# Optimization experiments

Measured on AMD Instinct MI355X. Metric: run time of the kernel, lower is better.

The kernel has to match this reference:

```python
import jax, jax.numpy as jnp
import numpy as np

# dims: batch, seq, d_model, heads, n_buckets, n_hashes, d_ff
B, S, D, H, NB, R, DFF = 2, 4096, 1024, 16, 64, 4, 4096
DH = D // H          # head dim
C = S // NB          # attention chunk length after bucket sort
NCH = S // C         # number of chunks


def layernorm(x, g, b):
    m = x.mean(-1, keepdims=True)
    v = ((x - m) ** 2).mean(-1, keepdims=True)
    return (x - m) / jnp.sqrt(v + 1e-5) * g + b


def lsh_attention(x, Wqk, Wv, Wo, rot):
    Bx, Sx, _ = x.shape
    # shared QK projection (Reformer-style), separate V
    qk = (x @ Wqk).reshape(Bx, Sx, H, DH).transpose(0, 2, 1, 3)  # [B,H,S,dh]
    v = (x @ Wv).reshape(Bx, Sx, H, DH).transpose(0, 2, 1, 3)
    # random-rotation LSH: rot [dh, R, NB//2]
    rotated = jnp.einsum('bhsd,drk->rbhsk', qk, rot)
    buckets = jnp.argmax(jnp.concatenate([rotated, -rotated], -1), -1)  # [R,B,H,S]
    scale = DH ** -0.5
    pos = jnp.arange(Sx)

    def one_round(b_r):  # b_r: [B,H,S] bucket ids for one hash round
        order = jnp.argsort(b_r * Sx + pos, axis=-1)   # stable sort by bucket
        inv = jnp.argsort(order, axis=-1)
        sqk = jnp.take_along_axis(qk, order[..., None], 2)
        sv = jnp.take_along_axis(v, order[..., None], 2)
        sb = jnp.take_along_axis(b_r, order, -1)
        q_c = sqk.reshape(Bx, H, NCH, C, DH)
        # keys are L2-normalized shared qk
        k_c = (sqk / (jnp.linalg.norm(sqk, axis=-1, keepdims=True) + 1e-6)).reshape(Bx, H, NCH, C, DH)
        v_c = sv.reshape(Bx, H, NCH, C, DH)
        ext = lambda t: jnp.concatenate([t, jnp.roll(t, 1, axis=2)], axis=3)  # look back 1 chunk
        k_e, v_e = ext(k_c), ext(v_c)
        b_c = sb.reshape(Bx, H, NCH, C)
        b_e = jnp.concatenate([b_c, jnp.roll(b_c, 1, axis=2)], 3)
        p_c = order.reshape(Bx, H, NCH, C)
        p_e = jnp.concatenate([p_c, jnp.roll(p_c, 1, axis=2)], 3)
        s = jnp.einsum('bhnqd,bhnkd->bhnqk', q_c, k_e) * scale  # [B,H,nch,C,2C]
        s = jnp.where(b_c[..., :, None] == b_e[..., None, :], s, -1e9)   # only same bucket
        s = jnp.where(p_c[..., :, None] == p_e[..., None, :], -1e5, s)   # discourage self
        l = jax.scipy.special.logsumexp(s, -1)
        o = jnp.einsum('bhnqk,bhnkd->bhnqd', jax.nn.softmax(s, -1), v_e)
        o = o.reshape(Bx, H, Sx, DH)
        l = l.reshape(Bx, H, Sx)
        return jnp.take_along_axis(o, inv[..., None], 2), jnp.take_along_axis(l, inv, -1)

    o_all, l_all = jax.vmap(one_round)(buckets)        # [R,B,H,S,dh], [R,B,H,S]
    w = jax.nn.softmax(l_all, axis=0)[..., None]       # weight rounds by logsumexp
    out = (o_all * w).sum(0).transpose(0, 2, 1, 3).reshape(Bx, Sx, D)
    return out @ Wo


def feedforward(x, W1, b1, W2, b2):
    # chunked FF in the original only tiles the sequence dim; math is identical
    return jax.nn.relu(x @ W1 + b1) @ W2 + b2


def setup_inputs() -> dict:
    key = jax.random.key(0)
    ks = jax.random.split(key, 10)
    n = jax.random.normal
    return {
        'x1': n(ks[0], (B, S, D), jnp.float32),
        'x2': n(ks[1], (B, S, D), jnp.float32),
        'Wqk': n(ks[2], (D, D), jnp.float32) * (D ** -0.5),
        'Wv': n(ks[3], (D, D), jnp.float32) * (D ** -0.5),
        'Wo': n(ks[4], (D, D), jnp.float32) * (D ** -0.5),
        'ln1_g': jnp.ones(D, jnp.float32), 'ln1_b': jnp.zeros(D, jnp.float32),
        'W1': n(ks[5], (D, DFF), jnp.float32) * (D ** -0.5), 'bf1': jnp.zeros(DFF, jnp.float32),
        'W2': n(ks[6], (DFF, D), jnp.float32) * (DFF ** -0.5), 'bf2': jnp.zeros(D, jnp.float32),
        'ln2_g': jnp.ones(D, jnp.float32), 'ln2_b': jnp.zeros(D, jnp.float32),
        'rot': n(ks[7], (DH, R, NB // 2), jnp.float32),
    }


def reference(x1, x2, Wqk, Wv, Wo, ln1_g, ln1_b, W1, bf1, W2, bf2, ln2_g, ln2_b, rot):
    # reversible block: y1 = x1 + Attn(LN(x2)); y2 = x2 + FF(LN(y1))
    y1 = x1 + lsh_attention(layernorm(x2, ln1_g, ln1_b), Wqk, Wv, Wo, rot)
    y2 = x2 + feedforward(layernorm(y1, ln2_g, ln2_b), W1, bf1, W2, bf2)
    return (y1, y2)
```

## Files before the change

kernel.cpp:

```cpp
#include <hip/hip_runtime.h>
#include <hip/hip_bf16.h>
#include <math.h>

constexpr int CB   = 2;
constexpr int CS   = 4096;
constexpr int CD   = 1024;
constexpr int CH   = 16;
constexpr int CDH  = 64;
constexpr int CR   = 4;
constexpr int CC   = 64;
constexpr int CNCH = 64;
constexpr int CDFF = 4096;
constexpr int CBS  = CB * CS;
constexpr int CBHS = CB * CH * CS;

typedef __attribute__((ext_vector_type(8))) short short8;
typedef __attribute__((ext_vector_type(4))) short short4v;
typedef __attribute__((ext_vector_type(4))) float f32x4;

__device__ inline unsigned short f2bf(float f) {
    __bf16 h = (__bf16)f;
    union { __bf16 h; unsigned short u; } c; c.h = h;
    return c.u;
}
__device__ inline unsigned int cvt2(float a, float b) {
    return (unsigned int)f2bf(a) | ((unsigned int)f2bf(b) << 16);
}
__device__ inline float bf2f(unsigned short h) {
    union { float f; unsigned int u; } a; a.u = ((unsigned int)h) << 16; return a.f;
}

#define AS3 __attribute__((address_space(3)))
#define AS1 __attribute__((address_space(1)))
__device__ inline void gload16(const unsigned short* g, unsigned short* l) {
    __builtin_amdgcn_global_load_lds((const AS1 unsigned int*)g,
                                     (AS3 unsigned int*)l, 16, 0, 0);
}

__device__ inline short8 ld_short8_u(const unsigned short* p) {
    short4v a = *(const short4v*)p;
    short4v b = *(const short4v*)(p + 4);
    short8 r;
    r[0] = a[0]; r[1] = a[1]; r[2] = a[2]; r[3] = a[3];
    r[4] = b[0]; r[5] = b[1]; r[6] = b[2]; r[7] = b[3];
    return r;
}

__global__ __launch_bounds__(256) void ln_kernel(const float* __restrict__ x,
        const float* __restrict__ g, const float* __restrict__ bta,
        unsigned short* __restrict__ out16, unsigned short* __restrict__ out16lo) {
    int row = blockIdx.x;
    int t = threadIdx.x;
    const float* xr = x + (size_t)row * CD;
    float4 v = *(const float4*)(xr + t * 4);
    float s  = v.x + v.y + v.z + v.w;
    float ss = v.x * v.x + v.y * v.y + v.z * v.z + v.w * v.w;
    #pragma unroll
    for (int off = 1; off < 64; off <<= 1) {
        s  += __shfl_xor(s, off);
        ss += __shfl_xor(ss, off);
    }
    __shared__ float ws_[4], wss_[4];
    int wid = t >> 6;
    if ((t & 63) == 0) { ws_[wid] = s; wss_[wid] = ss; }
    __syncthreads();
    s  = ws_[0] + ws_[1] + ws_[2] + ws_[3];
    ss = wss_[0] + wss_[1] + wss_[2] + wss_[3];
    float mean = s * (1.0f / CD);
    float var  = ss * (1.0f / CD) - mean * mean;
    float rstd = rsqrtf(var + 1e-5f);
    float4 gv = *(const float4*)(g + t * 4);
    float4 bv = *(const float4*)(bta + t * 4);
    float4 o;
    o.x = (v.x - mean) * rstd * gv.x + bv.x;
    o.y = (v.y - mean) * rstd * gv.y + bv.y;
    o.z = (v.z - mean) * rstd * gv.z + bv.z;
    o.w = (v.w - mean) * rstd * gv.w + bv.w;
    ushort4 h; h.x = f2bf(o.x); h.y = f2bf(o.y); h.z = f2bf(o.z); h.w = f2bf(o.w);
    *(ushort4*)(out16 + (size_t)row * CD + t * 4) = h;
    if (out16lo) {
        ushort4 lo;
        lo.x = f2bf(o.x - bf2f(h.x)); lo.y = f2bf(o.y - bf2f(h.y));
        lo.z = f2bf(o.z - bf2f(h.z)); lo.w = f2bf(o.w - bf2f(h.w));
        *(ushort4*)(out16lo + (size_t)row * CD + t * 4) = lo;
    }
}

__global__ __launch_bounds__(256) void wtrans_kernel(const float* __restrict__ W,
        unsigned short* __restrict__ WT, unsigned short* __restrict__ WTlo,
        int K, int N) {
    __shared__ float tile[64][65];
    int n0 = blockIdx.x * 64, k0 = blockIdx.y * 64;
    int tid = threadIdx.x;
    int r = tid >> 4, c4 = tid & 15;
    #pragma unroll
    for (int it = 0; it < 4; ++it) {
        int row = r + it * 16;
        float4 v = *(const float4*)(W + (size_t)(k0 + row) * N + n0 + c4 * 4);
        tile[row][c4 * 4 + 0] = v.x; tile[row][c4 * 4 + 1] = v.y;
        tile[row][c4 * 4 + 2] = v.z; tile[row][c4 * 4 + 3] = v.w;
    }
    __syncthreads();
    #pragma unroll
    for (int it = 0; it < 4; ++it) {
        int nrow = r + it * 16;
        float f0 = tile[c4 * 4 + 0][nrow], f1 = tile[c4 * 4 + 1][nrow];
        float f2 = tile[c4 * 4 + 2][nrow], f3 = tile[c4 * 4 + 3][nrow];
        ushort4 h;
        h.x = f2bf(f0); h.y = f2bf(f1); h.z = f2bf(f2); h.w = f2bf(f3);
        *(ushort4*)(WT + (size_t)(n0 + nrow) * K + k0 + c4 * 4) = h;
        if (WTlo) {
            ushort4 lo;
            lo.x = f2bf(f0 - bf2f(h.x)); lo.y = f2bf(f1 - bf2f(h.y));
            lo.z = f2bf(f2 - bf2f(h.z)); lo.w = f2bf(f3 - bf2f(h.w));
            *(ushort4*)(WTlo + (size_t)(n0 + nrow) * K + k0 + c4 * 4) = lo;
        }
    }
}

template<int EPI, int BM, int BK>
__global__ __launch_bounds__(256) void gemm_bf16(const unsigned short* __restrict__ A,
        const unsigned short* __restrict__ BT, const float* __restrict__ bias,
        const float* __restrict__ res, void* __restrict__ outp,
        int M, int N, int K) {
    constexpr int NH  = BK / 32;
    constexpr int SA  = BM / 64;
    constexpr int MI2 = BM / 32;
    __shared__ __align__(16) unsigned short As[NH * BM * 32];
    __shared__ __align__(16) unsigned short Bs[NH * 128 * 32];
    int tid = threadIdx.x;
    int w = tid >> 6, l = tid & 63;
    int nwg = gridDim.x * gridDim.y;
    int lid = blockIdx.y * gridDim.x + blockIdx.x;
    if (!(nwg & 7)) lid = (lid & 7) * (nwg >> 3) + (lid >> 3);
    int m0 = (lid / gridDim.x) * BM, n0 = (lid % gridDim.x) * 128;
    int wm = (w >> 1) * (BM / 2), wn = (w & 1) * 64;

    const unsigned short* gA[SA]; const unsigned short* gB[2];
    unsigned short* ldsA[SA]; unsigned short* ldsB[2];
    int gchunk = (l & 3) ^ ((l >> 3) & 3);
    #pragma unroll
    for (int s = 0; s < SA; ++s) {
        int j = w * SA + s;
        int R = j * 16 + (l >> 2);
        gA[s] = A + (size_t)(m0 + R) * K + gchunk * 8;
        ldsA[s] = As + j * 512;
    }
    #pragma unroll
    for (int s = 0; s < 2; ++s) {
        int j = w * 2 + s;
        int R = j * 16 + (l >> 2);
        gB[s] = BT + (size_t)(n0 + R) * K + gchunk * 8;
        ldsB[s] = Bs + j * 512;
    }
    int p = (l >> 4) ^ (((l & 15) >> 1) & 3);
    int aoff = (wm + (l & 15)) * 32 + p * 8;
    int boff = (wn + (l & 15)) * 32 + p * 8;

    f32x4 acc[MI2][4];
    #pragma unroll
    for (int i = 0; i < MI2; i++)
        #pragma unroll
        for (int j = 0; j < 4; j++) acc[i][j] = (f32x4)(0.f);

    for (int k0 = 0; k0 < K; k0 += BK) {
        #pragma unroll
        for (int h = 0; h < NH; ++h) {
            #pragma unroll
            for (int s = 0; s < SA; ++s)
                gload16(gA[s] + k0 + h * 32, ldsA[s] + h * (BM * 32));
            gload16(gB[0] + k0 + h * 32, ldsB[0] + h * (128 * 32));
            gload16(gB[1] + k0 + h * 32, ldsB[1] + h * (128 * 32));
        }
        __syncthreads();
        #pragma unroll
        for (int h = 0; h < NH; ++h) {
            short8 af[MI2], bf[4];
            #pragma unroll
            for (int im = 0; im < MI2; ++im)
                af[im] = *(const short8*)(As + h * (BM * 32) + aoff + im * 512);
            #pragma unroll
            for (int in = 0; in < 4; ++in)
                bf[in] = *(const short8*)(Bs + h * (128 * 32) + boff + in * 512);
            #pragma unroll
            for (int im = 0; im < MI2; ++im)
                #pragma unroll
                for (int in = 0; in < 4; ++in)
                    acc[im][in] = __builtin_amdgcn_mfma_f32_16x16x32_bf16(
                        af[im], bf[in], acc[im][in], 0, 0, 0);
        }
        __syncthreads();
    }

    float bv[4];
    if (EPI == 1 || EPI == 2) {
        #pragma unroll
        for (int in = 0; in < 4; ++in) bv[in] = bias[n0 + wn + in * 16 + (l & 15)];
    }
    #pragma unroll
    for (int im = 0; im < MI2; ++im) {
        #pragma unroll
        for (int in = 0; in < 4; ++in) {
            int n = n0 + wn + in * 16 + (l & 15);
            #pragma unroll
            for (int r = 0; r < 4; ++r) {
                int m = m0 + wm + im * 16 + (l >> 4) * 4 + r;
                float v = acc[im][in][r];
                if (EPI == 1) {
                    v = fmaxf(v + bv[in], 0.f);
                    ((unsigned short*)outp)[(size_t)m * N + n] = f2bf(v);
                } else if (EPI == 5) {
                    ((unsigned short*)outp)[(size_t)m * N + n] = f2bf(v);
                } else {
                    if (EPI == 2) v += bv[in] + res[(size_t)m * N + n];
                    if (EPI == 3) v += res[(size_t)m * N + n];
                    ((float*)outp)[(size_t)m * N + n] = v;
                }
            }
        }
    }
}

template<int BM>
__global__ __launch_bounds__(256) void gemm_bf16split(
        const unsigned short* __restrict__ Ah, const unsigned short* __restrict__ Al,
        const unsigned short* __restrict__ BTh, const unsigned short* __restrict__ BTl,
        float* __restrict__ outp, unsigned short* __restrict__ out16,
        int M, int N, int K) {
    constexpr int SA  = BM / 64;
    constexpr int MI2 = BM / 32;
    __shared__ __align__(16) unsigned short Ash[BM * 32];
    __shared__ __align__(16) unsigned short Asl[BM * 32];
    __shared__ __align__(16) unsigned short Bsh[128 * 32];
    __shared__ __align__(16) unsigned short Bsl[128 * 32];
    int tid = threadIdx.x;
    int w = tid >> 6, l = tid & 63;
    int nwg = gridDim.x * gridDim.y;
    int lid = blockIdx.y * gridDim.x + blockIdx.x;
    if (!(nwg & 7)) lid = (lid & 7) * (nwg >> 3) + (lid >> 3);
    int m0 = (lid / gridDim.x) * BM, n0 = (lid % gridDim.x) * 128;
    int wm = (w >> 1) * (BM / 2), wn = (w & 1) * 64;

    size_t goffA[SA]; size_t goffB[2];
    unsigned short* ldsAh[SA]; unsigned short* ldsAl[SA];
    unsigned short* ldsBh[2]; unsigned short* ldsBl[2];
    int gchunk = (l & 3) ^ ((l >> 3) & 3);
    #pragma unroll
    for (int s = 0; s < SA; ++s) {
        int j = w * SA + s;
        int R = j * 16 + (l >> 2);
        goffA[s] = (size_t)(m0 + R) * K + gchunk * 8;
        ldsAh[s] = Ash + j * 512; ldsAl[s] = Asl + j * 512;
    }
    #pragma unroll
    for (int s = 0; s < 2; ++s) {
        int j = w * 2 + s;
        int R = j * 16 + (l >> 2);
        goffB[s] = (size_t)(n0 + R) * K + gchunk * 8;
        ldsBh[s] = Bsh + j * 512; ldsBl[s] = Bsl + j * 512;
    }
    int p = (l >> 4) ^ (((l & 15) >> 1) & 3);
    int aoff = (wm + (l & 15)) * 32 + p * 8;
    int boff = (wn + (l & 15)) * 32 + p * 8;

    f32x4 acc[MI2][4];
    #pragma unroll
    for (int i = 0; i < MI2; i++)
        #pragma unroll
        for (int j = 0; j < 4; j++) acc[i][j] = (f32x4)(0.f);

    for (int k0 = 0; k0 < K; k0 += 32) {
        #pragma unroll
        for (int s = 0; s < SA; ++s) {
            gload16(Ah + goffA[s] + k0, ldsAh[s]);
            gload16(Al + goffA[s] + k0, ldsAl[s]);
        }
        #pragma unroll
        for (int s = 0; s < 2; ++s) {
            gload16(BTh + goffB[s] + k0, ldsBh[s]);
            gload16(BTl + goffB[s] + k0, ldsBl[s]);
        }
        __syncthreads();
        short8 afh[MI2], afl[MI2], bfh[4], bfl[4];
        #pragma unroll
        for (int im = 0; im < MI2; ++im) {
            afh[im] = *(const short8*)(Ash + aoff + im * 512);
            afl[im] = *(const short8*)(Asl + aoff + im * 512);
        }
        #pragma unroll
        for (int in = 0; in < 4; ++in) {
            bfh[in] = *(const short8*)(Bsh + boff + in * 512);
            bfl[in] = *(const short8*)(Bsl + boff + in * 512);
        }
        #pragma unroll
        for (int im = 0; im < MI2; ++im)
            #pragma unroll
            for (int in = 0; in < 4; ++in) {
                acc[im][in] = __builtin_amdgcn_mfma_f32_16x16x32_bf16(
                    afh[im], bfh[in], acc[im][in], 0, 0, 0);
                acc[im][in] = __builtin_amdgcn_mfma_f32_16x16x32_bf16(
                    afl[im], bfh[in], acc[im][in], 0, 0, 0);
                acc[im][in] = __builtin_amdgcn_mfma_f32_16x16x32_bf16(
                    afh[im], bfl[in], acc[im][in], 0, 0, 0);
            }
        __syncthreads();
    }

    #pragma unroll
    for (int im = 0; im < MI2; ++im)
        #pragma unroll
        for (int in = 0; in < 4; ++in) {
            int n = n0 + wn + in * 16 + (l & 15);
            #pragma unroll
            for (int r = 0; r < 4; ++r) {
                int m = m0 + wm + im * 16 + (l >> 4) * 4 + r;
                float v = acc[im][in][r];
                outp[(size_t)m * N + n] = v;
                out16[(size_t)m * N + n] = f2bf(v);
            }
        }
}

template<int EPI>
__global__ __launch_bounds__(256) void gemm_f32(const float* __restrict__ A,
        const float* __restrict__ W, float* __restrict__ out,
        int M, int N, int K) {
    __shared__ __align__(16) float As[16][132];
    __shared__ __align__(16) float Bs[16][132];
    int tid = threadIdx.x;
    int n0 = blockIdx.x * 128;
    int m0 = blockIdx.y * 128;
    int ty = tid >> 4, tx = tid & 15;
    float acc[8][8];
    #pragma unroll
    for (int i = 0; i < 8; i++)
        #pragma unroll
        for (int j = 0; j < 8; j++) acc[i][j] = 0.f;

    for (int k0 = 0; k0 < K; k0 += 16) {
        #pragma unroll
        for (int it = 0; it < 2; ++it) {
            int f4 = tid + it * 256;
            int row = f4 >> 2, c4 = f4 & 3;
            float4 av = *(const float4*)(A + (size_t)(m0 + row) * K + k0 + c4 * 4);
            As[c4 * 4 + 0][row] = av.x;
            As[c4 * 4 + 1][row] = av.y;
            As[c4 * 4 + 2][row] = av.z;
            As[c4 * 4 + 3][row] = av.w;
        }
        #pragma unroll
        for (int it = 0; it < 2; ++it) {
            int f4 = tid + it * 256;
            int kr = f4 >> 5, c4 = f4 & 31;
            *(float4*)(&Bs[kr][c4 * 4]) =
                *(const float4*)(W + (size_t)(k0 + kr) * N + n0 + c4 * 4);
        }
        __syncthreads();
        #pragma unroll
        for (int kk = 0; kk < 16; ++kk) {
            float4 a0 = *(const float4*)(&As[kk][ty * 8]);
            float4 a1 = *(const float4*)(&As[kk][ty * 8 + 4]);
            float4 b0 = *(const float4*)(&Bs[kk][tx * 8]);
            float4 b1 = *(const float4*)(&Bs[kk][tx * 8 + 4]);
            float am[8] = {a0.x, a0.y, a0.z, a0.w, a1.x, a1.y, a1.z, a1.w};
            float bn[8] = {b0.x, b0.y, b0.z, b0.w, b1.x, b1.y, b1.z, b1.w};
            #pragma unroll
            for (int i = 0; i < 8; i++)
                #pragma unroll
                for (int j = 0; j < 8; j++)
                    acc[i][j] = fmaf(am[i], bn[j], acc[i][j]);
        }
        __syncthreads();
    }

    if (EPI == 4) {
        int* ibuck = (int*)out;
        int q = tx & 3, r = tx >> 2;
        #pragma unroll
        for (int i = 0; i < 8; i++) {
            int m = m0 + ty * 8 + i;
            float bestP = -3.4e38f, bestN = -3.4e38f;
            int biP = 0, biN = 0;
            #pragma unroll
            for (int j = 0; j < 8; j++) {
                float v = acc[i][j];
                if ( v > bestP) { bestP =  v; biP = q * 8 + j; }
                if (-v > bestN) { bestN = -v; biN = q * 8 + j; }
            }
            #pragma unroll
            for (int off = 1; off < 4; off <<= 1) {
                float oP = __shfl_xor(bestP, off); int oiP = __shfl_xor(biP, off);
                float oN = __shfl_xor(bestN, off); int oiN = __shfl_xor(biN, off);
                if (oP > bestP || (oP == bestP && oiP < biP)) { bestP = oP; biP = oiP; }
                if (oN > bestN || (oN == bestN && oiN < biN)) { bestN = oN; biN = oiN; }
            }
            if (q == 0) {
                int bi = (bestP >= bestN) ? biP : (biN + 32);
                int hh = m & 15, ss2 = (m >> 4) & (CS - 1), bb2 = m >> 16;
                ibuck[((size_t)((r * CB + bb2) * CH + hh)) * CS + ss2] = bi;
            }
        }
        return;
    }

    #pragma unroll
    for (int i = 0; i < 8; i++) {
        int m = m0 + ty * 8 + i;
        #pragma unroll
        for (int j4 = 0; j4 < 2; j4++) {
            int n = n0 + tx * 8 + j4 * 4;
            float4 v;
            v.x = acc[i][j4 * 4 + 0]; v.y = acc[i][j4 * 4 + 1];
            v.z = acc[i][j4 * 4 + 2]; v.w = acc[i][j4 * 4 + 3];
            *(float4*)(out + (size_t)m * N + n) = v;
        }
    }
}

__global__ __launch_bounds__(64) void sort_kernel(const int* __restrict__ buckets,
                                                  int* __restrict__ sorted_pos) {
    int g = blockIdx.x;
    const int* bk = buckets + (size_t)g * CS;
    __shared__ int hist[64][65];
    __shared__ int bstart[64];
    int t = threadIdx.x;
    #pragma unroll
    for (int i = 0; i < 64; i++) hist[t][i] = 0;
    __syncthreads();
    int base = t * 64;
    for (int i = 0; i < 64; i++) { int b = bk[base + i]; hist[t][b]++; }
    __syncthreads();
    int run = 0;
    for (int tt = 0; tt < 64; tt++) {
        int c = hist[tt][t];
        hist[tt][t] = run;
        run += c;
    }
    int x = run;
    #pragma unroll
    for (int off = 1; off < 64; off <<= 1) {
        int y = __shfl_up(x, off);
        if (t >= off) x += y;
    }
    bstart[t] = x - run;
    __syncthreads();
    for (int i = 0; i < 64; i++) {
        int b = bk[base + i];
        int rank = bstart[b] + hist[t][b];
        hist[t][b]++;
        sorted_pos[(size_t)g * CS + rank] = base + i;
    }
}

__global__ __launch_bounds__(256) void attn_kernel(const unsigned short* __restrict__ qk16,
        const unsigned short* __restrict__ v16, const int* __restrict__ buckets,
        const int* __restrict__ sorted, unsigned short* __restrict__ o_all,
        float* __restrict__ l_all) {
    int n  = blockIdx.x;
    int r  = blockIdx.y;
    int bh = blockIdx.z;
    int b = bh >> 4, h = bh & 15;
    int rbh = (r * CB + b) * CH + h;
    int tid = threadIdx.x;
    int w = tid >> 6, l = tid & 63;
    int l4 = l & 15, qd = l >> 4;

    __shared__ int pk[128];
    __shared__ int bkk[128];
    __shared__ __align__(16) unsigned short Ks[128 * 72];
    __shared__ __align__(16) unsigned short Ps[64 * 132];
    __shared__ __align__(16) unsigned short VsT[64 * 132];

    int prev = (n + CNCH - 1) & (CNCH - 1);
    if (tid < 128) {
        int i = tid & 63;
        int ch = (tid < 64) ? n : prev;
        int p = sorted[(size_t)rbh * CS + ch * CC + i];
        pk[tid] = p;
        bkk[tid] = buckets[(size_t)rbh * CS + p];
    }
    __syncthreads();

    const unsigned short* qbase = qk16 + (size_t)b * CS * CD + h * 64;
    const unsigned short* vbase = v16  + (size_t)b * CS * CD + h * 64;

    #pragma unroll
    for (int it = 0; it < 8; ++it) {
        int f4 = tid + it * 256;
        int kk = f4 >> 4, d4 = f4 & 15;
        ushort4 hv = *(const ushort4*)(qbase + (size_t)pk[kk] * CD + d4 * 4);
        float x0 = bf2f(hv.x), x1 = bf2f(hv.y), x2 = bf2f(hv.z), x3 = bf2f(hv.w);
        float ss = x0 * x0 + x1 * x1 + x2 * x2 + x3 * x3;
        ss += __shfl_xor(ss, 1); ss += __shfl_xor(ss, 2);
        ss += __shfl_xor(ss, 4); ss += __shfl_xor(ss, 8);
        float rn = __builtin_amdgcn_rcpf(sqrtf(ss) + 1e-6f);
        uint2 kp;
        kp.x = cvt2(x0 * rn, x1 * rn);
        kp.y = cvt2(x2 * rn, x3 * rn);
        *(uint2*)&Ks[kk * 72 + d4 * 4] = kp;
    }
    #pragma unroll
    for (int it = 0; it < 16; ++it) {
        int kkp = w * 16 + it;
        int r0 = pk[2 * kkp], r1 = pk[2 * kkp + 1];
        unsigned int u0 = vbase[(size_t)r0 * CD + l];
        unsigned int u1 = vbase[(size_t)r1 * CD + l];
        *(unsigned int*)&VsT[l * 132 + 2 * kkp] = u0 | (u1 << 16);
    }
    int mstrip = w * 16;
    const unsigned short* qptr = qbase + (size_t)pk[mstrip + l4] * CD + qd * 8;
    short8 afA = *(const short8*)(qptr);
    short8 afB = *(const short8*)(qptr + 32);
    __syncthreads();

    f32x4 sa[8];
    #pragma unroll
    for (int t = 0; t < 8; ++t) sa[t] = (f32x4)(0.f);
    #pragma unroll
    for (int t = 0; t < 8; ++t) {
        const unsigned short* kb = &Ks[(t * 16 + l4) * 72 + qd * 8];
        short8 b0 = *(const short8*)(kb);
        short8 b1 = *(const short8*)(kb + 32);
        sa[t] = __builtin_amdgcn_mfma_f32_16x16x32_bf16(afA, b0, sa[t], 0, 0, 0);
        sa[t] = __builtin_amdgcn_mfma_f32_16x16x32_bf16(afB, b1, sa[t], 0, 0, 0);
    }

    int rowb[4], rowp[4];
    #pragma unroll
    for (int rr = 0; rr < 4; ++rr) {
        int m = mstrip + 4 * qd + rr;
        rowb[rr] = bkk[m]; rowp[rr] = pk[m];
    }
    float mx[4] = {-3.4e38f, -3.4e38f, -3.4e38f, -3.4e38f};
    #pragma unroll
    for (int t = 0; t < 8; ++t) {
        int cb = bkk[t * 16 + l4], cp = pk[t * 16 + l4];
        #pragma unroll
        for (int rr = 0; rr < 4; ++rr) {
            float v = sa[t][rr] * 0.125f;
            if (rowb[rr] != cb) v = -1e9f;
            if (rowp[rr] == cp) v = -1e5f;
            sa[t][rr] = v;
            mx[rr] = fmaxf(mx[rr], v);
        }
    }
    #pragma unroll
    for (int rr = 0; rr < 4; ++rr) {
        mx[rr] = fmaxf(mx[rr], __shfl_xor(mx[rr], 1));
        mx[rr] = fmaxf(mx[rr], __shfl_xor(mx[rr], 2));
        mx[rr] = fmaxf(mx[rr], __shfl_xor(mx[rr], 4));
        mx[rr] = fmaxf(mx[rr], __shfl_xor(mx[rr], 8));
    }
    float sum[4] = {0.f, 0.f, 0.f, 0.f};
    #pragma unroll
    for (int t = 0; t < 8; ++t)
        #pragma unroll
        for (int rr = 0; rr < 4; ++rr) {
            float e = __expf(sa[t][rr] - mx[rr]);
            sa[t][rr] = e;
            sum[rr] += e;
        }
    #pragma unroll
    for (int rr = 0; rr < 4; ++rr) {
        sum[rr] += __shfl_xor(sum[rr], 1);
        sum[rr] += __shfl_xor(sum[rr], 2);
        sum[rr] += __shfl_xor(sum[rr], 4);
        sum[rr] += __shfl_xor(sum[rr], 8);
    }
    if (l4 == 0) {
        #pragma unroll
        for (int rr = 0; rr < 4; ++rr)
            l_all[(size_t)rbh * CS + rowp[rr]] = mx[rr] + __logf(sum[rr]);
    }

    float rs[4];
    #pragma unroll
    for (int rr = 0; rr < 4; ++rr) rs[rr] = __builtin_amdgcn_rcpf(sum[rr]);
    #pragma unroll
    for (int t = 0; t < 8; ++t) {
        unsigned int a01 = cvt2(sa[t][0] * rs[0], sa[t][1] * rs[1]);
        unsigned int a23 = cvt2(sa[t][2] * rs[2], sa[t][3] * rs[3]);
        int base = (mstrip + 4 * qd) * 132 + t * 16 + l4;
        Ps[base]       = (unsigned short)(a01 & 0xffffu);
        Ps[base + 132] = (unsigned short)(a01 >> 16);
        Ps[base + 264] = (unsigned short)(a23 & 0xffffu);
        Ps[base + 396] = (unsigned short)(a23 >> 16);
    }

    f32x4 oa[4];
    #pragma unroll
    for (int nt = 0; nt < 4; ++nt) oa[nt] = (f32x4)(0.f);
    #pragma unroll
    for (int ks = 0; ks < 4; ++ks) {
        short8 ap = ld_short8_u(&Ps[(mstrip + l4) * 132 + ks * 32 + qd * 8]);
        #pragma unroll
        for (int nt = 0; nt < 4; ++nt) {
            short8 bv = ld_short8_u(&VsT[(nt * 16 + l4) * 132 + ks * 32 + qd * 8]);
            oa[nt] = __builtin_amdgcn_mfma_f32_16x16x32_bf16(ap, bv, oa[nt], 0, 0, 0);
        }
    }
    size_t ob = (size_t)rbh * CS;
    #pragma unroll
    for (int nt = 0; nt < 4; ++nt) {
        unsigned int a01 = cvt2(oa[nt][0], oa[nt][1]);
        unsigned int a23 = cvt2(oa[nt][2], oa[nt][3]);
        o_all[(ob + rowp[0]) * CDH + nt * 16 + l4] = (unsigned short)(a01 & 0xffffu);
        o_all[(ob + rowp[1]) * CDH + nt * 16 + l4] = (unsigned short)(a01 >> 16);
        o_all[(ob + rowp[2]) * CDH + nt * 16 + l4] = (unsigned short)(a23 & 0xffffu);
        o_all[(ob + rowp[3]) * CDH + nt * 16 + l4] = (unsigned short)(a23 >> 16);
    }
}

__global__ __launch_bounds__(256) void combine_kernel(const unsigned short* __restrict__ o_all,
        const float* __restrict__ l_all, unsigned short* __restrict__ attnout16) {
    int idx = blockIdx.x * 256 + threadIdx.x;
    int d = idx & 63, bhs = idx >> 6;
    int s2 = bhs & (CS - 1), bh = bhs >> 12, h = bh & 15, b = bh >> 4;
    float lr[4];
    #pragma unroll
    for (int r = 0; r < CR; r++) lr[r] = l_all[(size_t)r * CBHS + bhs];
    float m = fmaxf(fmaxf(lr[0], lr[1]), fmaxf(lr[2], lr[3]));
    float w[4], sum = 0.f;
    #pragma unroll
    for (int r = 0; r < CR; r++) { w[r] = __expf(lr[r] - m); sum += w[r]; }
    float acc = 0.f;
    #pragma unroll
    for (int r = 0; r < CR; r++)
        acc += w[r] * bf2f(o_all[((size_t)r * CBHS + bhs) * CDH + d]);
    acc *= __builtin_amdgcn_rcpf(sum);
    attnout16[((size_t)(b * CS + s2)) * CD + h * 64 + d] = f2bf(acc);
}

extern "C" void kernel_launch(void* const* d_in, const int* in_sizes, int n_in,
                              void* d_out, int out_size, void* d_ws, size_t ws_size,
                              hipStream_t stream) {
    const float* x1   = (const float*)d_in[0];
    const float* x2   = (const float*)d_in[1];
    const float* Wqk  = (const float*)d_in[2];
    const float* Wv   = (const float*)d_in[3];
    const float* Wo   = (const float*)d_in[4];
    const float* ln1g = (const float*)d_in[5];
    const float* ln1b = (const float*)d_in[6];
    const float* W1   = (const float*)d_in[7];
    const float* bf1  = (const float*)d_in[8];
    const float* W2   = (const float*)d_in[9];
    const float* bf2  = (const float*)d_in[10];
    const float* ln2g = (const float*)d_in[11];
    const float* ln2b = (const float*)d_in[12];
    const float* rot  = (const float*)d_in[13];

    unsigned short* bufA16   = (unsigned short*)d_ws;
    unsigned short* bufA16lo = bufA16 + (size_t)CBS * CD;
    float* bufB = (float*)(bufA16lo + (size_t)CBS * CD);
    float* bufC = bufB + (size_t)CBS * CD;
    unsigned short* v16  = (unsigned short*)bufC;
    unsigned short* qk16 = v16 + (size_t)CBS * CD;
    unsigned short* o_all = (unsigned short*)(bufC + (size_t)CBS * CD);
    float* l_all  = (float*)(o_all + (size_t)CR * CBHS * CDH);
    int* buckets  = (int*)(l_all + (size_t)CR * CBHS);
    int* sorted   = buckets + (size_t)CR * CBHS;
    unsigned short* WvT   = (unsigned short*)(sorted + (size_t)CR * CBHS);
    unsigned short* WoT   = WvT + (size_t)CD * CD;
    unsigned short* W1T   = WoT + (size_t)CD * CD;
    unsigned short* W2T   = W1T + (size_t)CD * CDFF;
    unsigned short* WqkTh = W2T + (size_t)CD * CDFF;
    unsigned short* WqkTl = WqkTh + (size_t)CD * CD;
    unsigned short* ffh16 = (unsigned short*)bufB;
    unsigned short* attnout16 = bufA16;
    unsigned short* lnY16 = bufA16;
    float* y1 = (float*)d_out;
    float* y2 = y1 + (size_t)CBS * CD;

    wtrans_kernel<<<dim3(CD / 64, CD / 64), 256, 0, stream>>>(Wqk, WqkTh, WqkTl, CD, CD);
    wtrans_kernel<<<dim3(CD / 64, CD / 64), 256, 0, stream>>>(Wv, WvT, nullptr, CD, CD);
    wtrans_kernel<<<dim3(CD / 64, CD / 64), 256, 0, stream>>>(Wo, WoT, nullptr, CD, CD);
    wtrans_kernel<<<dim3(CDFF / 64, CD / 64), 256, 0, stream>>>(W1, W1T, nullptr, CD, CDFF);
    wtrans_kernel<<<dim3(CD / 64, CDFF / 64), 256, 0, stream>>>(W2, W2T, nullptr, CDFF, CD);
    ln_kernel<<<CBS, 256, 0, stream>>>(x2, ln1g, ln1b, bufA16, bufA16lo);
    gemm_bf16split<64><<<dim3(CD / 128, CBS / 64), 256, 0, stream>>>(
        bufA16, bufA16lo, WqkTh, WqkTl, bufB, qk16, CBS, CD, CD);
    gemm_bf16<5, 64, 64><<<dim3(CD / 128, CBS / 64), 256, 0, stream>>>(
        bufA16, WvT, nullptr, nullptr, v16, CBS, CD, CD);
    gemm_f32<4><<<dim3(1, CBHS / 128), 256, 0, stream>>>(bufB, rot, (float*)buckets, CBHS, 128, 64);
    sort_kernel<<<CR * CB * CH, 64, 0, stream>>>(buckets, sorted);
    attn_kernel<<<dim3(CNCH, CR, CB * CH), 256, 0, stream>>>(qk16, v16, buckets, sorted, o_all, l_all);
    combine_kernel<<<(CBHS * CDH) / 256, 256, 0, stream>>>(o_all, l_all, attnout16);
    gemm_bf16<3, 64, 64><<<dim3(CD / 128, CBS / 64), 256, 0, stream>>>(
        attnout16, WoT, nullptr, x1, y1, CBS, CD, CD);
    ln_kernel<<<CBS, 256, 0, stream>>>(y1, ln2g, ln2b, lnY16, nullptr);
    gemm_bf16<1, 128, 32><<<dim3(CDFF / 128, CBS / 128), 256, 0, stream>>>(
        lnY16, W1T, bf1, nullptr, ffh16, CBS, CDFF, CD);
    gemm_bf16<2, 64, 64><<<dim3(CD / 128, CBS / 64), 256, 0, stream>>>(
        ffh16, W2T, bf2, x2, y2, CBS, CD, CDFF);
}
```

Measured before the change: 643.3 us.

## Split-K the FF2 GEMM with larger tiles and a separate combine kernel

The second feed-forward GEMM changes from 64x128 tiles running over the full K range to 128x128 tiles with K split in two across gridDim.z. Each split writes fp32 partial sums into the reused attention scratch buffer. A new elementwise kernel then adds the two partials, the bias and the residual x2 to produce y2. The larger tiles aim to improve operand reuse while keeping the workgroup count the same, at the cost of extra fp32 partial-sum traffic and one more kernel launch.

Result: slower. 670.0 us (+4.1%).

```diff
diff --git a/kernel.cpp b/kernel.cpp
--- a/kernel.cpp
+++ b/kernel.cpp
@@ -135,6 +135,8 @@
     if (!(nwg & 7)) lid = (lid & 7) * (nwg >> 3) + (lid >> 3);
     int m0 = (lid / gridDim.x) * BM, n0 = (lid % gridDim.x) * 128;
     int wm = (w >> 1) * (BM / 2), wn = (w & 1) * 64;
+    int kn = K / gridDim.z;
+    int kbeg = blockIdx.z * kn;
 
     const unsigned short* gA[SA]; const unsigned short* gB[2];
     unsigned short* ldsA[SA]; unsigned short* ldsB[2];
@@ -163,7 +165,7 @@
         #pragma unroll
         for (int j = 0; j < 4; j++) acc[i][j] = (f32x4)(0.f);
 
-    for (int k0 = 0; k0 < K; k0 += BK) {
+    for (int k0 = kbeg; k0 < kbeg + kn; k0 += BK) {
         #pragma unroll
         for (int h = 0; h < NH; ++h) {
             #pragma unroll
@@ -197,6 +199,8 @@
         #pragma unroll
         for (int in = 0; in < 4; ++in) bv[in] = bias[n0 + wn + in * 16 + (l & 15)];
     }
+    float* pout = (float*)outp;
+    if (EPI == 6) pout += (size_t)blockIdx.z * M * N;
     #pragma unroll
     for (int im = 0; im < MI2; ++im) {
         #pragma unroll
@@ -214,11 +218,28 @@
                 } else {
                     if (EPI == 2) v += bv[in] + res[(size_t)m * N + n];
                     if (EPI == 3) v += res[(size_t)m * N + n];
-                    ((float*)outp)[(size_t)m * N + n] = v;
+                    pout[(size_t)m * N + n] = v;
                 }
             }
         }
     }
+}
+
+__global__ __launch_bounds__(256) void ff2_combine(const float* __restrict__ P,
+        const float* __restrict__ bias, const float* __restrict__ res,
+        float* __restrict__ y2) {
+    size_t idx = ((size_t)blockIdx.x * 256 + threadIdx.x) * 4;
+    int n = (int)(idx & (CD - 1));
+    float4 p0 = *(const float4*)(P + idx);
+    float4 p1 = *(const float4*)(P + (size_t)CBS * CD + idx);
+    float4 bv = *(const float4*)(bias + n);
+    float4 rv = *(const float4*)(res + idx);
+    float4 o;
+    o.x = p0.x + p1.x + bv.x + rv.x;
+    o.y = p0.y + p1.y + bv.y + rv.y;
+    o.z = p0.z + p1.z + bv.z + rv.z;
+    o.w = p0.w + p1.w + bv.w + rv.w;
+    *(float4*)(y2 + idx) = o;
 }
 
 template<int BM>
@@ -668,6 +689,7 @@
     unsigned short* ffh16 = (unsigned short*)bufB;
     unsigned short* attnout16 = bufA16;
     unsigned short* lnY16 = bufA16;
+    float* ff2P = (float*)o_all;
     float* y1 = (float*)d_out;
     float* y2 = y1 + (size_t)CBS * CD;
 
@@ -690,6 +712,7 @@
     ln_kernel<<<CBS, 256, 0, stream>>>(y1, ln2g, ln2b, lnY16, nullptr);
     gemm_bf16<1, 128, 32><<<dim3(CDFF / 128, CBS / 128), 256, 0, stream>>>(
         lnY16, W1T, bf1, nullptr, ffh16, CBS, CDFF, CD);
-    gemm_bf16<2, 64, 64><<<dim3(CD / 128, CBS / 64), 256, 0, stream>>>(
-        ffh16, W2T, bf2, x2, y2, CBS, CD, CDFF);
-}
+    gemm_bf16<6, 128, 32><<<dim3(CD / 128, CBS / 128, 2), 256, 0, stream>>>(
+        ffh16, W2T, nullptr, nullptr, ff2P, CBS, CD, CDFF);
+    ff2_combine<<<(CBS * CD) / 1024, 256, 0, stream>>>(ff2P, bf2, x2, y2);
+}
```

## Add triple-buffered LDS pipeline to BM64 bf16 GEMMs

Applied to the files above, without the earlier changes.

Adds a PIPE mode to the bf16 GEMM that keeps three LDS buffers, prefetching the tile two K-steps ahead while computing the current one. It waits with a manual vmcnt and a single barrier per iteration instead of two full __syncthreads. The V, Wo and W2 GEMMs switch to BK=32 with this pipeline; the W1 GEMM keeps the old path. This is meant to hide global-load latency behind MFMA work, but the hand-written vmcnt literal depends on the load count per stage, and the smaller BK means more loop iterations.

New measurement: 657.7 us. +2.2%, slower.

```diff
diff --git a/kernel.cpp b/kernel.cpp
--- a/kernel.cpp
+++ b/kernel.cpp
@@ -118,7 +118,7 @@
     }
 }
 
-template<int EPI, int BM, int BK>
+template<int EPI, int BM, int BK, int PIPE>
 __global__ __launch_bounds__(256) void gemm_bf16(const unsigned short* __restrict__ A,
         const unsigned short* __restrict__ BT, const float* __restrict__ bias,
         const float* __restrict__ res, void* __restrict__ outp,
@@ -126,8 +126,12 @@
     constexpr int NH  = BK / 32;
     constexpr int SA  = BM / 64;
     constexpr int MI2 = BM / 32;
-    __shared__ __align__(16) unsigned short As[NH * BM * 32];
-    __shared__ __align__(16) unsigned short Bs[NH * 128 * 32];
+    constexpr int NBUF = PIPE ? 3 : 1;
+    constexpr int ASZ = NH * BM * 32;
+    constexpr int BSZ = NH * 128 * 32;
+    static_assert(!PIPE || (BM == 64 && BK == 32), "PIPE tuned for BM64/BK32 (vmcnt literal = 3)");
+    __shared__ __align__(16) unsigned short As[NBUF * ASZ];
+    __shared__ __align__(16) unsigned short Bs[NBUF * BSZ];
     int tid = threadIdx.x;
     int w = tid >> 6, l = tid & 63;
     int nwg = gridDim.x * gridDim.y;
@@ -163,25 +167,26 @@
         #pragma unroll
         for (int j = 0; j < 4; j++) acc[i][j] = (f32x4)(0.f);
 
-    for (int k0 = 0; k0 < K; k0 += BK) {
+    auto STAGE = [&](int buf, int k0) {
         #pragma unroll
         for (int h = 0; h < NH; ++h) {
             #pragma unroll
             for (int s = 0; s < SA; ++s)
-                gload16(gA[s] + k0 + h * 32, ldsA[s] + h * (BM * 32));
-            gload16(gB[0] + k0 + h * 32, ldsB[0] + h * (128 * 32));
-            gload16(gB[1] + k0 + h * 32, ldsB[1] + h * (128 * 32));
-        }
-        __syncthreads();
+                gload16(gA[s] + k0 + h * 32, ldsA[s] + buf * ASZ + h * (BM * 32));
+            gload16(gB[0] + k0 + h * 32, ldsB[0] + buf * BSZ + h * (128 * 32));
+            gload16(gB[1] + k0 + h * 32, ldsB[1] + buf * BSZ + h * (128 * 32));
+        }
+    };
+    auto COMPUTE = [&](int buf) {
         #pragma unroll
         for (int h = 0; h < NH; ++h) {
             short8 af[MI2], bf[4];
             #pragma unroll
             for (int im = 0; im < MI2; ++im)
-                af[im] = *(const short8*)(As + h * (BM * 32) + aoff + im * 512);
+                af[im] = *(const short8*)(As + buf * ASZ + h * (BM * 32) + aoff + im * 512);
             #pragma unroll
             for (int in = 0; in < 4; ++in)
-                bf[in] = *(const short8*)(Bs + h * (128 * 32) + boff + in * 512);
+                bf[in] = *(const short8*)(Bs + buf * BSZ + h * (128 * 32) + boff + in * 512);
             #pragma unroll
             for (int im = 0; im < MI2; ++im)
                 #pragma unroll
@@ -189,7 +194,38 @@
                     acc[im][in] = __builtin_amdgcn_mfma_f32_16x16x32_bf16(
                         af[im], bf[in], acc[im][in], 0, 0, 0);
         }
-        __syncthreads();
+    };
+
+    if (PIPE) {
+        STAGE(0, 0);
+        STAGE(1, BK);
+        asm volatile("s_waitcnt vmcnt(3)" ::: "memory");
+        __builtin_amdgcn_s_barrier();
+        asm volatile("" ::: "memory");
+        int cur = 0;
+        for (int k0 = 0; k0 < K; k0 += BK) {
+            bool stg = (k0 + 2 * BK < K);
+            if (stg) {
+                int nxt = cur + 2; if (nxt >= 3) nxt -= 3;
+                STAGE(nxt, k0 + 2 * BK);
+            }
+            COMPUTE(cur);
+            if (stg) {
+                asm volatile("s_waitcnt vmcnt(3)" ::: "memory");
+            } else {
+                asm volatile("s_waitcnt vmcnt(0)" ::: "memory");
+            }
+            __builtin_amdgcn_s_barrier();
+            asm volatile("" ::: "memory");
+            ++cur; if (cur >= 3) cur = 0;
+        }
+    } else {
+        for (int k0 = 0; k0 < K; k0 += BK) {
+            STAGE(0, k0);
+            __syncthreads();
+            COMPUTE(0);
+            __syncthreads();
+        }
     }
 
     float bv[4];
@@ -679,17 +715,17 @@
     ln_kernel<<<CBS, 256, 0, stream>>>(x2, ln1g, ln1b, bufA16, bufA16lo);
     gemm_bf16split<64><<<dim3(CD / 128, CBS / 64), 256, 0, stream>>>(
         bufA16, bufA16lo, WqkTh, WqkTl, bufB, qk16, CBS, CD, CD);
-    gemm_bf16<5, 64, 64><<<dim3(CD / 128, CBS / 64), 256, 0, stream>>>(
+    gemm_bf16<5, 64, 32, 1><<<dim3(CD / 128, CBS / 64), 256, 0, stream>>>(
         bufA16, WvT, nullptr, nullptr, v16, CBS, CD, CD);
     gemm_f32<4><<<dim3(1, CBHS / 128), 256, 0, stream>>>(bufB, rot, (float*)buckets, CBHS, 128, 64);
     sort_kernel<<<CR * CB * CH, 64, 0, stream>>>(buckets, sorted);
     attn_kernel<<<dim3(CNCH, CR, CB * CH), 256, 0, stream>>>(qk16, v16, buckets, sorted, o_all, l_all);
     combine_kernel<<<(CBHS * CDH) / 256, 256, 0, stream>>>(o_all, l_all, attnout16);
-    gemm_bf16<3, 64, 64><<<dim3(CD / 128, CBS / 64), 256, 0, stream>>>(
+    gemm_bf16<3, 64, 32, 1><<<dim3(CD / 128, CBS / 64), 256, 0, stream>>>(
         attnout16, WoT, nullptr, x1, y1, CBS, CD, CD);
     ln_kernel<<<CBS, 256, 0, stream>>>(y1, ln2g, ln2b, lnY16, nullptr);
-    gemm_bf16<1, 128, 32><<<dim3(CDFF / 128, CBS / 128), 256, 0, stream>>>(
+    gemm_bf16<1, 128, 32, 0><<<dim3(CDFF / 128, CBS / 128), 256, 0, stream>>>(
         lnY16, W1T, bf1, nullptr, ffh16, CBS, CDFF, CD);
-    gemm_bf16<2, 64, 64><<<dim3(CD / 128, CBS / 64), 256, 0, stream>>>(
+    gemm_bf16<2, 64, 32, 1><<<dim3(CD / 128, CBS / 64), 256, 0, stream>>>(
         ffh16, W2T, bf2, x2, y2, CBS, CD, CDFF);
 }
```
